# Kernel optimization log

Measured on AMD Instinct MI355X. Metric: run time of the kernel, lower is better.

The kernel has to match this reference:

```python
import jax, jax.numpy as jnp
import numpy as np

B, L, D, H = 4, 2048, 1024, 16
HD = D // H


def setup_inputs() -> dict:
    key = jax.random.key(0)
    k1, k2, k3 = jax.random.split(key, 3)
    # xavier_uniform bounds for Linear(d, 3d) and Linear(d, d)
    b_qkv = float(np.sqrt(6.0 / (D + 3 * D)))
    b_out = float(np.sqrt(6.0 / (D + D)))
    x = jax.random.normal(k1, (B, L, D), dtype=jnp.float32)
    W_qkv = jax.random.uniform(k2, (3 * D, D), dtype=jnp.float32, minval=-b_qkv, maxval=b_qkv)
    W_out = jax.random.uniform(k3, (D, D), dtype=jnp.float32, minval=-b_out, maxval=b_out)
    return {"x": x, "W_qkv": W_qkv, "W_out": W_out}


def reference(x, W_qkv, W_out):
    b, l, d = x.shape
    # fused QKV projection: [B,L,3d] -> [3,B,H,L,Hd]
    qkv = (x @ W_qkv.T).reshape(b, l, 3, H, HD).transpose(2, 0, 3, 1, 4)
    q, k, v = qkv[0], qkv[1], qkv[2]
    # naive causal attention: full [B,H,L,L] score matrix, as in the original
    scores = jnp.einsum('bhqd,bhkd->bhqk', q, k) / (HD ** 0.5)
    mask = jnp.tril(jnp.ones((l, l), dtype=bool))  # causal mask recomputed per call
    scores = jnp.where(mask, scores, -jnp.inf)
    attn = jax.nn.softmax(scores, axis=-1)
    ctx = jnp.einsum('bhqk,bhkd->bhqd', attn, v)          # [B,H,L,Hd]
    ctx = ctx.transpose(0, 2, 1, 3).reshape(b, l, d)       # [B,L,d]
    return ctx @ W_out.T
```

## Files before the change

kernel.cpp:

```cpp
#include <hip/hip_runtime.h>

#define BB 4
#define LL 2048
#define DD 1024
#define HH 16
#define HD 64

typedef __attribute__((ext_vector_type(8))) short s16x8;
typedef __attribute__((ext_vector_type(4))) short s16x4;
typedef __attribute__((ext_vector_type(4))) float f32x4;

#define SCALE_LOG2E 0.18033688011112042f

__device__ __forceinline__ short f2bf(float f) {
  union { float f; unsigned u; } c;
  c.f = f;
  return (short)((c.u + 0x7fffu + ((c.u >> 16) & 1u)) >> 16);
}

__device__ __forceinline__ void cp16(const void* g, void* l) {
  __builtin_amdgcn_global_load_lds(
      (const __attribute__((address_space(1))) void*)g,
      (__attribute__((address_space(3))) void*)l, 16, 0, 0);
}

__global__ __launch_bounds__(256) void f2b_all(const float* __restrict__ x,
                                               const float* __restrict__ wqkv,
                                               const float* __restrict__ wout,
                                               short* __restrict__ xb,
                                               short* __restrict__ wqkvb,
                                               short* __restrict__ woutb) {
  const int bid = blockIdx.x;
  const float* in;
  short* out;
  int i0;
  if (bid < 8192) {
    in = x; out = xb; i0 = bid;
  } else if (bid < 8192 + 3072) {
    in = wqkv; out = wqkvb; i0 = bid - 8192;
  } else {
    in = wout; out = woutb; i0 = bid - (8192 + 3072);
  }
  const int i = i0 * 256 + threadIdx.x;
  float4 v = ((const float4*)in)[i];
  s16x4 o;
  o[0] = f2bf(v.x);
  o[1] = f2bf(v.y);
  o[2] = f2bf(v.z);
  o[3] = f2bf(v.w);
  ((s16x4*)out)[i] = o;
}

template <int MODE>
__global__ __launch_bounds__(256, 3) void gemm_bt(const short* __restrict__ A,
                                                  const short* __restrict__ Bm,
                                                  int K, int N,
                                                  short* __restrict__ qo,
                                                  short* __restrict__ ko,
                                                  short* __restrict__ vo,
                                                  float* __restrict__ fo) {
  __shared__ __align__(16) short As[3][128 * 32];
  __shared__ __align__(16) short Bs[3][128 * 32];
  const int tid = threadIdx.x;
  const int m0 = blockIdx.y * 128, n0 = blockIdx.x * 128;
  const int wave = tid >> 6, lane = tid & 63;
  const int quad = lane >> 4, c16 = lane & 15;
  const int wr = (wave >> 1) * 64, wc = (wave & 1) * 64;

  f32x4 zero = {0.f, 0.f, 0.f, 0.f};
  f32x4 acc[4][4];
#pragma unroll
  for (int i = 0; i < 4; i++)
#pragma unroll
    for (int j = 0; j < 4; j++) acc[i][j] = zero;

  const int row1 = tid >> 2;
  const int gsw = ((tid & 3) ^ ((tid >> 3) & 3)) * 8;
  const short* Ag = A + (size_t)(m0 + row1) * K + gsw;
  const short* Bg = Bm + (size_t)(n0 + row1) * K + gsw;
  const int rsw = (quad ^ ((c16 >> 1) & 3)) * 8;

  auto stage = [&](int t, int bi) {
    const int k0 = t << 5;
    cp16(Ag + k0, As[bi] + wave * 512);
    cp16(Ag + (size_t)64 * K + k0, As[bi] + 2048 + wave * 512);
    cp16(Bg + k0, Bs[bi] + wave * 512);
    cp16(Bg + (size_t)64 * K + k0, Bs[bi] + 2048 + wave * 512);
  };

  const int T = K >> 5;
  stage(0, 0);
  stage(1, 1);
  asm volatile("s_waitcnt vmcnt(4)" ::: "memory");
  __builtin_amdgcn_s_barrier();
  asm volatile("" ::: "memory");

  int bcur = 0;
  for (int t = 0; t < T; t++) {
    const short* Asb = As[bcur];
    const short* Bsb = Bs[bcur];
    s16x8 af[4], bfv[4];
#pragma unroll
    for (int i = 0; i < 4; i++)
      af[i] = *(const s16x8*)&Asb[(wr + i * 16 + c16) * 32 + rsw];
#pragma unroll
    for (int j = 0; j < 4; j++)
      bfv[j] = *(const s16x8*)&Bsb[(wc + j * 16 + c16) * 32 + rsw];
    if (t + 2 < T) {
      int b2 = bcur + 2;
      if (b2 >= 3) b2 -= 3;
      stage(t + 2, b2);
    }
    __builtin_amdgcn_s_setprio(1);
#pragma unroll
    for (int i = 0; i < 4; i++)
#pragma unroll
      for (int j = 0; j < 4; j++)
        acc[i][j] = __builtin_amdgcn_mfma_f32_16x16x32_bf16(af[i], bfv[j], acc[i][j], 0, 0, 0);
    __builtin_amdgcn_s_setprio(0);
    if (t < T - 2) asm volatile("s_waitcnt vmcnt(4)" ::: "memory");
    else if (t == T - 2) asm volatile("s_waitcnt vmcnt(0)" ::: "memory");
    __builtin_amdgcn_s_barrier();
    asm volatile("" ::: "memory");
    bcur = (bcur == 2) ? 0 : bcur + 1;
  }

  if (MODE == 0) {
#pragma unroll
    for (int j = 0; j < 4; j++) {
      const int gn = n0 + wc + j * 16 + c16;
      const int which = gn >> 10;
      const int h = (gn >> 6) & 15;
      const int hd = gn & 63;
      if (which == 2) {
#pragma unroll
        for (int i = 0; i < 4; i++) {
          const int gm = m0 + wr + i * 16 + quad * 4;
          const int b = gm >> 11, l = gm & 2047;
          s16x4 vv;
#pragma unroll
          for (int r = 0; r < 4; r++) vv[r] = f2bf(acc[i][j][r]);
          *(s16x4*)&vo[((size_t)((b << 4) + h) * HD + hd) * LL + l] = vv;
        }
      } else {
        short* dst = which == 0 ? qo : ko;
        const float sc = which == 0 ? SCALE_LOG2E : 1.0f;
#pragma unroll
        for (int i = 0; i < 4; i++)
#pragma unroll
          for (int r = 0; r < 4; r++) {
            const int gm = m0 + wr + i * 16 + quad * 4 + r;
            const int b = gm >> 11, l = gm & 2047;
            dst[((size_t)((b << 4) + h) * LL + l) * HD + hd] = f2bf(acc[i][j][r] * sc);
          }
      }
    }
  } else {
#pragma unroll
    for (int i = 0; i < 4; i++)
#pragma unroll
      for (int r = 0; r < 4; r++) {
        const int gm = m0 + wr + i * 16 + quad * 4 + r;
#pragma unroll
        for (int j = 0; j < 4; j++) {
          const int gn = n0 + wc + j * 16 + c16;
          fo[(size_t)gm * N + gn] = acc[i][j][r];
        }
      }
  }
}

__global__ __launch_bounds__(512, 4) void attn_kernel(const short* __restrict__ Qb,
                                                      const short* __restrict__ Kb,
                                                      const short* __restrict__ Vtb,
                                                      short* __restrict__ Cb) {
  const int pi = blockIdx.x;
  const int bh = blockIdx.y;
  const int tid = threadIdx.x;
  const int wave = tid >> 6, lane = tid & 63;
  const int quad = lane >> 4, c16 = lane & 15;
  const int sw = c16 & 7;
  const size_t base = (size_t)bh * LL * HD;
  const short* Q = Qb + base;
  const short* K = Kb + base;
  const short* Vt = Vtb + base;

  __shared__ __align__(16) short Ks[2][128 * 64];
  __shared__ __align__(16) short Vs[2][64 * 128];

  const f32x4 zero = {0.f, 0.f, 0.f, 0.f};
  const s16x4 ones = {(short)0x3F80, (short)0x3F80, (short)0x3F80, (short)0x3F80};

  const int k_r = lane >> 3, k_c = lane & 7;
  const int v_r = lane >> 4, v_c = lane & 15;
  const int ksw = (k_c ^ k_r) * 8;
  const int vsw = (v_c ^ ((wave * 4 + v_r) & 15)) * 8;
  auto stage = [&](int kb, int bi) {
#pragma unroll
    for (int i = 0; i < 2; i++) {
      const int gk = i * 64 + wave * 8 + k_r;
      cp16(K + (size_t)(kb + gk) * HD + ksw, &Ks[bi][(i * 64 + wave * 8) * 64]);
      const int gv = i * 32 + wave * 4 + v_r;
      cp16(Vt + (size_t)gv * LL + kb + vsw, &Vs[bi][(i * 32 + wave * 4) * 128]);
    }
  };

  auto pack4 = [&](const float* p) {
    union { float f; unsigned u; } a0, a1, a2, a3;
    a0.f = p[0]; a1.f = p[1]; a2.f = p[2]; a3.f = p[3];
    union { s16x4 v; unsigned u[2]; } r;
    r.u[0] = __builtin_amdgcn_perm(a1.u, a0.u, 0x07060302u);
    r.u[1] = __builtin_amdgcn_perm(a3.u, a2.u, 0x07060302u);
    return r.v;
  };

  for (int phase = 0; phase < 2; phase++) {
    const int qg = phase == 0 ? (15 - pi) : pi;
    const int qw = qg * 128 + wave * 16;
    const int tiles = qg + 1;

    s16x8 qf[2];
#pragma unroll
    for (int s = 0; s < 2; s++)
      qf[s] = *(const s16x8*)(Q + (size_t)(qw + c16) * HD + s * 32 + quad * 8);

    f32x4 o[4];
#pragma unroll
    for (int j4 = 0; j4 < 4; j4++) o[j4] = zero;
    f32x4 ol = zero;

    stage(0, 0);
    __syncthreads();

    for (int t = 0; t < tiles; t++) {
      const int kb = t * 128;
      if (t + 1 < tiles) stage(kb + 128, (t + 1) & 1);
      const short* Kt = &Ks[t & 1][0];
      const short* Vv = &Vs[t & 1][0];

      const int D = qw - kb;
      const int jm = min((D >> 4) + 1, 8);
      const int jb = D >> 4;

#pragma unroll
      for (int j = 0; j < 8; j++) {
        if (j >= jm) continue;
        s16x8 kf0 = *(const s16x8*)&Kt[(j * 16 + c16) * 64 + ((quad ^ sw) * 8)];
        s16x8 kf1 = *(const s16x8*)&Kt[(j * 16 + c16) * 64 + (((4 + quad) ^ sw) * 8)];
        s16x4 va[4];
#pragma unroll
        for (int j4 = 0; j4 < 4; j4++)
          va[j4] = *(const s16x4*)&Vv[(j4 * 16 + c16) * 128 +
                                      (((2 * j + (quad >> 1)) ^ c16) * 8) + (quad & 1) * 4];
        f32x4 s = __builtin_amdgcn_mfma_f32_16x16x32_bf16(kf0, qf[0], zero, 0, 0, 0);
        s = __builtin_amdgcn_mfma_f32_16x16x32_bf16(kf1, qf[1], s, 0, 0, 0);
        float p[4];
#pragma unroll
        for (int r = 0; r < 4; r++) p[r] = __builtin_amdgcn_exp2f(s[r]);
        if (j == jb) {
          const int thr = c16 + D - j * 16 - quad * 4;
#pragma unroll
          for (int r = 0; r < 4; r++)
            if (r > thr) p[r] = 0.f;
        }
        s16x4 pb = pack4(p);
        ol = __builtin_amdgcn_mfma_f32_16x16x16bf16_1k(ones, pb, ol, 0, 0, 0);
#pragma unroll
        for (int j4 = 0; j4 < 4; j4++)
          o[j4] = __builtin_amdgcn_mfma_f32_16x16x16bf16_1k(va[j4], pb, o[j4], 0, 0, 0);
      }

      __syncthreads();
    }

    const int b = bh >> 4, h2 = bh & 15;
    const float inv = 1.0f / ol[0];
    const int q = qw + c16;
#pragma unroll
    for (int j4 = 0; j4 < 4; j4++) {
      s16x4 ov;
#pragma unroll
      for (int r = 0; r < 4; r++) ov[r] = f2bf(o[j4][r] * inv);
      *(s16x4*)&Cb[(size_t)(b * LL + q) * DD + h2 * HD + j4 * 16 + quad * 4] = ov;
    }
  }
}

extern "C" void kernel_launch(void* const* d_in, const int* in_sizes, int n_in,
                              void* d_out, int out_size, void* d_ws, size_t ws_size,
                              hipStream_t stream) {
  const float* x = (const float*)d_in[0];
  const float* wqkv = (const float*)d_in[1];
  const float* wout = (const float*)d_in[2];
  float* out = (float*)d_out;

  const size_t NX = (size_t)BB * LL * DD;
  short* xb = (short*)d_ws;
  short* wqkvb = xb + NX;
  short* woutb = wqkvb + (size_t)3 * DD * DD;
  short* qb = woutb + (size_t)DD * DD;
  short* kb = qb + NX;
  short* vb = kb + NX;
  short* cb = vb + NX;

  f2b_all<<<dim3(8192 + 3072 + 1024), 256, 0, stream>>>(x, wqkv, wout, xb, wqkvb, woutb);

  gemm_bt<0><<<dim3(3 * DD / 128, BB * LL / 128), 256, 0, stream>>>(
      xb, wqkvb, DD, 3 * DD, qb, kb, vb, nullptr);
  attn_kernel<<<dim3(8, BB * HH), 512, 0, stream>>>(qb, kb, vb, cb);
  gemm_bt<1><<<dim3(DD / 128, BB * LL / 128), 256, 0, stream>>>(
      cb, woutb, DD, DD, nullptr, nullptr, nullptr, out);
}
```

Before: 239.9 us.

## Load GEMM B operand straight from global into registers, bypassing LDS

In the bf16 GEMM, operand B is no longer staged through shared memory. Each wave now loads its own B fragments from global memory into registers one K-step ahead, double-buffered in registers by unrolling the loop by two. The A operand keeps its three-stage LDS pipeline, and the waitcnt thresholds are adjusted for the new mix of loads. This removes the B LDS buffers and the LDS reads for B, which may allow more blocks per CU. In exchange, the two waves that share B rows fetch them twice from global/L2, and only one step of register prefetch may not fully hide global-load latency.

```diff
diff --git a/kernel.cpp b/kernel.cpp
--- a/kernel.cpp
+++ b/kernel.cpp
@@ -60,7 +60,6 @@
                                                   short* __restrict__ vo,
                                                   float* __restrict__ fo) {
   __shared__ __align__(16) short As[3][128 * 32];
-  __shared__ __align__(16) short Bs[3][128 * 32];
   const int tid = threadIdx.x;
   const int m0 = blockIdx.y * 128, n0 = blockIdx.x * 128;
   const int wave = tid >> 6, lane = tid & 63;
@@ -77,52 +76,63 @@
   const int row1 = tid >> 2;
   const int gsw = ((tid & 3) ^ ((tid >> 3) & 3)) * 8;
   const short* Ag = A + (size_t)(m0 + row1) * K + gsw;
-  const short* Bg = Bm + (size_t)(n0 + row1) * K + gsw;
   const int rsw = (quad ^ ((c16 >> 1) & 3)) * 8;
 
-  auto stage = [&](int t, int bi) {
+  const short* Bg = Bm + (size_t)(n0 + wc + c16) * K + quad * 8;
+
+  auto stageA = [&](int t, int bi) {
     const int k0 = t << 5;
     cp16(Ag + k0, As[bi] + wave * 512);
     cp16(Ag + (size_t)64 * K + k0, As[bi] + 2048 + wave * 512);
-    cp16(Bg + k0, Bs[bi] + wave * 512);
-    cp16(Bg + (size_t)64 * K + k0, Bs[bi] + 2048 + wave * 512);
+  };
+  auto loadB = [&](int t, s16x8 (&bn)[4]) {
+#pragma unroll
+    for (int j = 0; j < 4; j++)
+      bn[j] = *(const s16x8*)(Bg + (size_t)(j * 16) * K + t * 32);
   };
 
   const int T = K >> 5;
-  stage(0, 0);
-  stage(1, 1);
-  asm volatile("s_waitcnt vmcnt(4)" ::: "memory");
+  s16x8 bA[4], bB[4];
+  loadB(0, bA);
+  stageA(0, 0);
+  stageA(1, 1);
+  asm volatile("s_waitcnt vmcnt(2)" ::: "memory");
   __builtin_amdgcn_s_barrier();
   asm volatile("" ::: "memory");
 
-  int bcur = 0;
-  for (int t = 0; t < T; t++) {
+  auto body = [&](int t, int bcur, s16x8 (&bc)[4], s16x8 (&bn)[4]) {
     const short* Asb = As[bcur];
-    const short* Bsb = Bs[bcur];
-    s16x8 af[4], bfv[4];
+    s16x8 af[4];
 #pragma unroll
     for (int i = 0; i < 4; i++)
       af[i] = *(const s16x8*)&Asb[(wr + i * 16 + c16) * 32 + rsw];
-#pragma unroll
-    for (int j = 0; j < 4; j++)
-      bfv[j] = *(const s16x8*)&Bsb[(wc + j * 16 + c16) * 32 + rsw];
+    if (t + 1 < T) loadB(t + 1, bn);
     if (t + 2 < T) {
       int b2 = bcur + 2;
       if (b2 >= 3) b2 -= 3;
-      stage(t + 2, b2);
+      stageA(t + 2, b2);
     }
     __builtin_amdgcn_s_setprio(1);
 #pragma unroll
     for (int i = 0; i < 4; i++)
 #pragma unroll
       for (int j = 0; j < 4; j++)
-        acc[i][j] = __builtin_amdgcn_mfma_f32_16x16x32_bf16(af[i], bfv[j], acc[i][j], 0, 0, 0);
+        acc[i][j] = __builtin_amdgcn_mfma_f32_16x16x32_bf16(af[i], bc[j], acc[i][j], 0, 0, 0);
     __builtin_amdgcn_s_setprio(0);
-    if (t < T - 2) asm volatile("s_waitcnt vmcnt(4)" ::: "memory");
-    else if (t == T - 2) asm volatile("s_waitcnt vmcnt(0)" ::: "memory");
-    __builtin_amdgcn_s_barrier();
-    asm volatile("" ::: "memory");
-    bcur = (bcur == 2) ? 0 : bcur + 1;
+    if (t < T - 2) asm volatile("s_waitcnt vmcnt(6)" ::: "memory");
+    else if (t == T - 2) asm volatile("s_waitcnt vmcnt(4)" ::: "memory");
+    if (t + 1 < T) {
+      __builtin_amdgcn_s_barrier();
+      asm volatile("" ::: "memory");
+    }
+  };
+
+  int bcur = 0;
+  for (int t = 0; t < T; t += 2) {
+    body(t, bcur, bA, bB);
+    bcur = (bcur >= 2) ? bcur - 2 : bcur + 1;
+    body(t + 1, bcur, bB, bA);
+    bcur = (bcur >= 2) ? bcur - 2 : bcur + 1;
   }
 
   if (MODE == 0) {
```

After: 304.0 us. +26.7%, slower.
